# Performance work log

Measured on AMD Instinct MI355X. Metric: run time of the kernel, lower is better.

## Reference

```python
import jax, jax.numpy as jnp
import numpy as np

D = 256; NH = 8; NL = 4; NP = 4; HD = D // NH
SHAPES = np.array([[180, 180], [90, 90], [45, 45], [23, 23]], dtype=np.int32)
LQ = int((SHAPES[:, 0] * SHAPES[:, 1]).sum())  # 43054
STARTS = np.concatenate([[0], np.cumsum(SHAPES[:, 0] * SHAPES[:, 1])[:-1]]).astype(np.int32)


def setup_inputs():
    ks = jax.random.split(jax.random.key(0), 16)
    s = 0.02
    p = lambda k, shp: jax.random.normal(k, shp, jnp.float32) * s
    return {
        "query": jax.random.normal(ks[0], (1, LQ, D), jnp.float32),
        "ref_points": jax.random.uniform(ks[1], (1, LQ, NL, 2), dtype=jnp.float32),
        "pos": jax.random.normal(ks[2], (1, LQ, D), jnp.float32),
        "input_spatial_shapes": jnp.asarray(SHAPES),
        "input_level_start_index": jnp.asarray(STARTS),
        "w_off": p(ks[3], (D, NH * NL * NP * 2)), "b_off": p(ks[4], (NH * NL * NP * 2,)),
        "w_attn": p(ks[5], (D, NH * NL * NP)), "b_attn": p(ks[6], (NH * NL * NP,)),
        "w_val": p(ks[7], (D, D)), "b_val": jnp.zeros((D,), jnp.float32),
        "w_out": p(ks[8], (D, D)), "b_out": jnp.zeros((D,), jnp.float32),
        "g1": jnp.ones((D,), jnp.float32), "beta1": jnp.zeros((D,), jnp.float32),
        "w1": p(ks[9], (D, D)), "b1": jnp.zeros((D,), jnp.float32),
        "w2": p(ks[10], (D, D)), "b2": jnp.zeros((D,), jnp.float32),
        "g2": jnp.ones((D,), jnp.float32), "beta2": jnp.zeros((D,), jnp.float32),
    }


def _ln(x, g, b):
    m = x.mean(-1, keepdims=True)
    v = ((x - m) ** 2).mean(-1, keepdims=True)
    return (x - m) * jax.lax.rsqrt(v + 1e-5) * g + b


def _sample_level(v, Hl, Wl, loc):
    # v: (B, Hl*Wl, NH, HD); loc: (B, Lq, NH, NP, 2) normalized to [0,1]
    # Bilinear sampling matching F.grid_sample(align_corners=False, padding_mode='zeros')
    B, _, nh, d = v.shape
    Lq, P = loc.shape[1], loc.shape[3]
    vb = jnp.transpose(v, (0, 2, 1, 3))  # (B, NH, HW, d)
    x = loc[..., 0] * Wl - 0.5
    y = loc[..., 1] * Hl - 0.5
    x0 = jnp.floor(x); y0 = jnp.floor(y)
    fx = x - x0; fy = y - y0
    out = jnp.zeros((B, nh, Lq, P, d), v.dtype)
    for dy in (0, 1):
        for dx in (0, 1):
            xi = x0 + dx; yi = y0 + dy
            w = (fx if dx else 1.0 - fx) * (fy if dy else 1.0 - fy)
            valid = (xi >= 0) & (xi < Wl) & (yi >= 0) & (yi < Hl)
            xc = jnp.clip(xi, 0, Wl - 1).astype(jnp.int32)
            yc = jnp.clip(yi, 0, Hl - 1).astype(jnp.int32)
            idx = jnp.transpose(yc * Wl + xc, (0, 2, 1, 3)).reshape(B, nh, Lq * P)
            g = jnp.take_along_axis(vb, idx[..., None], axis=2).reshape(B, nh, Lq, P, d)
            wt = jnp.transpose(jnp.where(valid, w, 0.0), (0, 2, 1, 3))
            out = out + g * wt[..., None]
    return out  # (B, NH, Lq, NP, HD)


def _layer(query, ref_points, pos, shp, sti, w_off, b_off, w_attn, b_attn, w_val, b_val,
           w_out, b_out, g1, beta1, w1, b1, w2, b2, g2, beta2):
    B, Lq, _ = query.shape
    q = query + pos  # with_pos_embed
    value = (query @ w_val + b_val).reshape(B, Lq, NH, HD)
    off = (q @ w_off + b_off).reshape(B, Lq, NH, NL, NP, 2)
    aw = jax.nn.softmax((q @ w_attn + b_attn).reshape(B, Lq, NH, NL * NP), axis=-1)
    aw = aw.reshape(B, Lq, NH, NL, NP)
    # offset_normalizer = [W_l, H_l]
    norm = jnp.asarray(shp[:, ::-1].copy(), jnp.float32)
    loc = ref_points[:, :, None, :, None, :] + off / norm[None, None, None, :, None, :]
    acc = jnp.zeros((B, NH, Lq, HD), query.dtype)
    for l in range(NL):
        Hl, Wl = int(shp[l, 0]), int(shp[l, 1])
        st = int(sti[l])
        sampled = _sample_level(value[:, st:st + Hl * Wl], Hl, Wl, loc[:, :, :, l])
        wl = jnp.transpose(aw[:, :, :, l], (0, 2, 1, 3))  # (B, NH, Lq, NP)
        acc = acc + (sampled * wl[..., None]).sum(axis=3)
    attn_out = acc.transpose(0, 2, 1, 3).reshape(B, Lq, D) @ w_out + b_out
    # residual + LayerNorm + FFN (dropout is identity in eval mode)
    x = _ln(query + attn_out, g1, beta1)
    ffn = jax.nn.relu(x @ w1 + b1) @ w2 + b2
    return _ln(x + ffn, g2, beta2)


def reference(query, ref_points, pos, input_spatial_shapes, input_level_start_index,
              w_off, b_off, w_attn, b_attn, w_val, b_val, w_out, b_out,
              g1, beta1, w1, b1, w2, b2, g2, beta2):
    shp = np.asarray(input_spatial_shapes)
    sti = np.asarray(input_level_start_index)
    return _layer(query, ref_points, pos, shp, sti, w_off, b_off, w_attn, b_attn,
                  w_val, b_val, w_out, b_out, g1, beta1, w1, b1, w2, b2, g2, beta2)
```

## Files before the change

kernel.cpp:

```cpp
#include <hip/hip_runtime.h>

typedef unsigned short u16;
typedef unsigned int u32;
typedef float f32x4 __attribute__((ext_vector_type(4)));
typedef short i16x8 __attribute__((ext_vector_type(8)));
typedef __bf16 bf16x8_t __attribute__((ext_vector_type(8)));

#define LQ 43054

__device__ __forceinline__ float bf2f(u16 u) {
  union { u32 i; float f; } v; v.i = ((u32)u) << 16; return v.f;
}
__device__ __forceinline__ u16 f2bf(float f) {
  u32 i = __float_as_uint(f);
  return (u16)((i + 0x7FFFu + ((i >> 16) & 1u)) >> 16);
}

__device__ __forceinline__ float dot2bf(u32 v, u32 w, float c) {
  float d;
  asm("v_dot2_f32_bf16 %0, %1, %2, %3" : "=v"(d) : "v"(v), "v"(w), "v"(c));
  return d;
}

template <typename T>
__device__ __forceinline__ auto mfma_try(T a, T b, f32x4 c, int)
    -> decltype(__builtin_amdgcn_mfma_f32_16x16x32_bf16(a, b, c, 0, 0, 0)) {
  return __builtin_amdgcn_mfma_f32_16x16x32_bf16(a, b, c, 0, 0, 0);
}
template <typename T>
__device__ __forceinline__ f32x4 mfma_try(T a, T b, f32x4 c, long) {
  return __builtin_amdgcn_mfma_f32_16x16x32_bf16(
      __builtin_bit_cast(bf16x8_t, a), __builtin_bit_cast(bf16x8_t, b), c, 0, 0, 0);
}
__device__ __forceinline__ f32x4 mfma_bf16(i16x8 a, i16x8 b, f32x4 c) {
  return mfma_try(a, b, c, 0);
}

__global__ void transpose_all_kernel(
    const float* __restrict__ w_off, const float* __restrict__ w_attn,
    const float* __restrict__ w_val, const float* __restrict__ w_out,
    const float* __restrict__ w1, const float* __restrict__ w2,
    u16* __restrict__ wT) {
  int b = blockIdx.x;
  const float* src; u16* dst; int N; int col;
  if (b < 256)       { src = w_off;  dst = wT;          N = 256; col = b; }
  else if (b < 384)  { src = w_attn; dst = wT + 65536;  N = 128; col = b - 256; }
  else if (b < 640)  { src = w_val;  dst = wT + 98304;  N = 256; col = b - 384; }
  else if (b < 896)  { src = w_out;  dst = wT + 163840; N = 256; col = b - 640; }
  else if (b < 1152) { src = w1;     dst = wT + 229376; N = 256; col = b - 896; }
  else               { src = w2;     dst = wT + 294912; N = 256; col = b - 1152; }
  dst[col * 256 + threadIdx.x] = f2bf(src[threadIdx.x * N + col]);
}

__device__ __forceinline__ void stage_a_dma(uint4* As, const u16* A, int r0, int M,
                                            int w, int lane) {
#pragma unroll
  for (int jj = 0; jj < 8; ++jj) {
    int row = w * 16 + jj * 2 + (lane >> 5);
    int gr = min(r0 + row, M - 1);
    int c = lane & 31;
    const uint4* gp = (const uint4*)A + (size_t)gr * 32 + (c ^ (row & 7));
    __builtin_amdgcn_global_load_lds(
        (const __attribute__((address_space(1))) void*)gp,
        (__attribute__((address_space(3))) void*)(As + (w * 16 + jj * 2) * 32),
        16, 0, 0);
  }
}
template <int ADD, int PH>
__device__ __forceinline__ void stage_a_f32(uint4* As, const float* A, const float* A2,
                                            int r0, int M, int tid) {
  constexpr int IT = 16 / PH;
#pragma unroll
  for (int h = 0; h < PH; ++h) {
    float4 va[IT];
    float4 vp[ADD ? IT : 1];
#pragma unroll
    for (int it = 0; it < IT; ++it) {
      int e = tid + (h * IT + it) * 256;
      int gr = min(r0 + (e >> 6), M - 1);
      int idx = gr * 64 + (e & 63);
      va[it] = ((const float4*)A)[idx];
      if constexpr (ADD) vp[it] = ((const float4*)A2)[idx];
    }
#pragma unroll
    for (int it = 0; it < IT; ++it) {
      int e = tid + (h * IT + it) * 256;
      int row = e >> 6, c4 = e & 63;
      float4 v = va[it];
      if constexpr (ADD) {
        v.x += vp[it].x; v.y += vp[it].y; v.z += vp[it].z; v.w += vp[it].w;
      }
      uint2 pk;
      pk.x = (u32)f2bf(v.x) | ((u32)f2bf(v.y) << 16);
      pk.y = (u32)f2bf(v.z) | ((u32)f2bf(v.w) << 16);
      int c = c4 >> 1, hf = c4 & 1;
      ((uint2*)As)[((row * 32 + (c ^ (row & 7))) << 1) | hf] = pk;
    }
  }
}
__device__ __forceinline__ void load_b(i16x8* f, const u16* Bt, int t, int l16, int quad) {
  const uint4* bp = (const uint4*)Bt + (t * 16 + l16) * 32 + quad;
#pragma unroll
  for (int kk = 0; kk < 8; ++kk) f[kk] = __builtin_bit_cast(i16x8, bp[kk << 2]);
}
__device__ __forceinline__ void tile_mfma(f32x4* acc, const uint4* As,
                                          const i16x8* bfr, int l16, int quad) {
#pragma unroll
  for (int rg = 0; rg < 4; ++rg) {
    int arow = rg * 16 + l16;
    f32x4 a = {0.f, 0.f, 0.f, 0.f};
#pragma unroll
    for (int kk = 0; kk < 8; ++kk) {
      i16x8 afr = __builtin_bit_cast(i16x8, As[arow * 32 + (((kk << 2) + quad) ^ (arow & 7))]);
      a = mfma_bf16(afr, bfr[kk], a);
    }
    acc[rg] = a;
  }
}

#define LS_STRIDE 264
__device__ __forceinline__ void lds_store_rows(const u16* Ls, u16* out,
                                               int r0, int M, int w, int lane) {
#pragma unroll
  for (int it = 0; it < 8; ++it) {
    int lrow = w * 16 + it * 2 + (lane >> 5);
    int grow = r0 + lrow;
    int chunk = lane & 31;
    if (grow < M) {
      *(uint4*)(out + (size_t)grow * 256 + chunk * 8) =
          *(const uint4*)(Ls + lrow * LS_STRIDE + chunk * 8);
    }
  }
}

template <int AIN, int MODE>
__global__ __launch_bounds__(256, 3) void gemm_kernel(
    const void* __restrict__ Av, const u16* __restrict__ Bt,
    const float* __restrict__ bias, void* __restrict__ out, int M) {
  __shared__ uint4 As[2176];
  const int tid = threadIdx.x;
  const int w = tid >> 6, lane = tid & 63, quad = lane >> 4, l16 = lane & 15;
  const int r0 = blockIdx.x * 64;
  if constexpr (AIN == 2) stage_a_dma(As, (const u16*)Av, r0, M, w, lane);
  else                    stage_a_f32<0, 2>(As, (const float*)Av, nullptr, r0, M, tid);
  __syncthreads();
  i16x8 bfr[2][8];
  load_b(bfr[0], Bt, w * 4, l16, quad);
  f32x4 vals[4][4];
#pragma unroll
  for (int i = 0; i < 4; ++i) {
    const int t = w * 4 + i;
    if (i + 1 < 4) load_b(bfr[(i + 1) & 1], Bt, t + 1, l16, quad);
    tile_mfma(vals[i], As, bfr[i & 1], l16, quad);
  }
  __syncthreads();
  u16* Ls = (u16*)As;
#pragma unroll
  for (int i = 0; i < 4; ++i) {
    const int col = (w * 4 + i) * 16 + l16;
    const float bv = bias[col];
#pragma unroll
    for (int rg = 0; rg < 4; ++rg)
#pragma unroll
      for (int r = 0; r < 4; ++r) {
        float v = vals[i][rg][r] + bv;
        if (MODE == 2) v = fmaxf(v, 0.f);
        Ls[(rg * 16 + (quad << 2) + r) * LS_STRIDE + col] = f2bf(v);
      }
  }
  __syncthreads();
  lds_store_rows(Ls, (u16*)out, r0, M, w, lane);
}

__global__ __launch_bounds__(256, 3) void offaw_gemm_kernel(
    const float* __restrict__ query, const float* __restrict__ pos,
    const u16* __restrict__ Bt, const float* __restrict__ b_off,
    const float* __restrict__ b_attn, u16* __restrict__ offb,
    float* __restrict__ aw, int M) {
  __shared__ uint4 As[2176];
  const int tid = threadIdx.x;
  const int w = tid >> 6, lane = tid & 63, quad = lane >> 4, l16 = lane & 15;
  const int r0 = blockIdx.x * 64;
  stage_a_f32<1, 4>(As, query, pos, r0, M, tid);
  __syncthreads();
  i16x8 bfr[2][8];
  load_b(bfr[0], Bt, w, l16, quad);
  f32x4 vals[4][4];
#pragma unroll
  for (int i = 0; i < 6; ++i) {
    const int t = w + 4 * i;
    if (i + 1 < 6) load_b(bfr[(i + 1) & 1], Bt, w + 4 * (i + 1), l16, quad);
    if (i < 4) {
      tile_mfma(vals[i], As, bfr[i & 1], l16, quad);
    } else {
      f32x4 acc[4];
      tile_mfma(acc, As, bfr[i & 1], l16, quad);
      const int colc = (t - 16) * 16 + l16;
      const float bv = b_attn[colc];
#pragma unroll
      for (int rg = 0; rg < 4; ++rg)
#pragma unroll
        for (int r = 0; r < 4; ++r) {
          float v = acc[rg][r] + bv;
          float m = v;
#pragma unroll
          for (int o = 1; o < 16; o <<= 1) m = fmaxf(m, __shfl_xor(m, o));
          float e = __expf(v - m);
          float s = e;
#pragma unroll
          for (int o = 1; o < 16; o <<= 1) s += __shfl_xor(s, o);
          int row = r0 + rg * 16 + (quad << 2) + r;
          if (row < M) aw[row * 128 + colc] = e / s;
        }
    }
  }
  __syncthreads();
  u16* Ls = (u16*)As;
#pragma unroll
  for (int i = 0; i < 4; ++i) {
    const int col = (w + 4 * i) * 16 + l16;
    const float bv = b_off[col];
#pragma unroll
    for (int rg = 0; rg < 4; ++rg)
#pragma unroll
      for (int r = 0; r < 4; ++r)
        Ls[(rg * 16 + (quad << 2) + r) * LS_STRIDE + col] = f2bf(vals[i][rg][r] + bv);
  }
  __syncthreads();
  lds_store_rows(Ls, offb, r0, M, w, lane);
}

template <int RBF, int OBF>
__global__ __launch_bounds__(256, 2) void gemm_ln_kernel(
    const u16* __restrict__ A, const u16* __restrict__ Bt,
    const float* __restrict__ bias, const void* __restrict__ residv,
    const float* __restrict__ g, const float* __restrict__ beta,
    void* __restrict__ outv, int M) {
  __shared__ uint4 As[2176];
  __shared__ float2 pnorm[256];
  const int tid = threadIdx.x;
  const int w = tid >> 6, lane = tid & 63, quad = lane >> 4, l16 = lane & 15;
  const int r0 = blockIdx.x * 64;
  stage_a_dma(As, A, r0, M, w, lane);
  __syncthreads();
  i16x8 bfr[2][8];
  load_b(bfr[0], Bt, w * 4, l16, quad);
  f32x4 vals[4][4];
#pragma unroll
  for (int i = 0; i < 4; ++i) {
    const int t = w * 4 + i;
    if (i + 1 < 4) load_b(bfr[(i + 1) & 1], Bt, t + 1, l16, quad);
    tile_mfma(vals[i], As, bfr[i & 1], l16, quad);
  }
  float s[16], s2[16];
#pragma unroll
  for (int k = 0; k < 16; ++k) { s[k] = 0.f; s2[k] = 0.f; }
#pragma unroll
  for (int i = 0; i < 4; ++i) {
    const int col = (w * 4 + i) * 16 + l16;
    const float bv = bias[col];
#pragma unroll
    for (int rg = 0; rg < 4; ++rg)
#pragma unroll
      for (int r = 0; r < 4; ++r) {
        int row = r0 + rg * 16 + (quad << 2) + r;
        float rv = 0.f;
        if (row < M) rv = RBF ? bf2f(((const u16*)residv)[row * 256 + col])
                              : ((const float*)residv)[row * 256 + col];
        float v = vals[i][rg][r] + bv + rv;
        vals[i][rg][r] = v;
        s[rg * 4 + r] += v; s2[rg * 4 + r] += v * v;
      }
  }
#pragma unroll
  for (int k = 0; k < 16; ++k)
#pragma unroll
    for (int o = 1; o < 16; o <<= 1) {
      s[k] += __shfl_xor(s[k], o);
      s2[k] += __shfl_xor(s2[k], o);
    }
  if (l16 == 0) {
#pragma unroll
    for (int rg = 0; rg < 4; ++rg)
#pragma unroll
      for (int r = 0; r < 4; ++r) {
        int lrow = rg * 16 + (quad << 2) + r;
        pnorm[lrow * 4 + w] = make_float2(s[rg * 4 + r], s2[rg * 4 + r]);
      }
  }
  __syncthreads();
  if constexpr (OBF) {
    u16* Ls = (u16*)As;
#pragma unroll
    for (int rg = 0; rg < 4; ++rg)
#pragma unroll
      for (int r = 0; r < 4; ++r) {
        int lrow = rg * 16 + (quad << 2) + r;
        float4 p01 = ((const float4*)pnorm)[lrow * 2];
        float4 p23 = ((const float4*)pnorm)[lrow * 2 + 1];
        float ss = p01.x + p01.z + p23.x + p23.z;
        float qq = p01.y + p01.w + p23.y + p23.w;
        float mean = ss * (1.f / 256.f);
        float var = qq * (1.f / 256.f) - mean * mean;
        float inv = rsqrtf(var + 1e-5f);
#pragma unroll
        for (int i = 0; i < 4; ++i) {
          const int col = (w * 4 + i) * 16 + l16;
          float o = (vals[i][rg][r] - mean) * inv * g[col] + beta[col];
          Ls[lrow * LS_STRIDE + col] = f2bf(o);
        }
      }
    __syncthreads();
    lds_store_rows(Ls, (u16*)outv, r0, M, w, lane);
  } else {
#pragma unroll
    for (int rg = 0; rg < 4; ++rg)
#pragma unroll
      for (int r = 0; r < 4; ++r) {
        int lrow = rg * 16 + (quad << 2) + r;
        float4 p01 = ((const float4*)pnorm)[lrow * 2];
        float4 p23 = ((const float4*)pnorm)[lrow * 2 + 1];
        float ss = p01.x + p01.z + p23.x + p23.z;
        float qq = p01.y + p01.w + p23.y + p23.w;
        float mean = ss * (1.f / 256.f);
        float var = qq * (1.f / 256.f) - mean * mean;
        float inv = rsqrtf(var + 1e-5f);
        int row = r0 + lrow;
        if (row < M) {
#pragma unroll
          for (int i = 0; i < 4; ++i) {
            const int col = (w * 4 + i) * 16 + l16;
            float o = (vals[i][rg][r] - mean) * inv * g[col] + beta[col];
            ((float*)outv)[row * 256 + col] = o;
          }
        }
      }
  }
}

__global__ __launch_bounds__(256) void sampler_kernel(
    const float* __restrict__ refp, const u16* __restrict__ offb,
    const float* __restrict__ aw, const u16* __restrict__ value,
    u32* __restrict__ accv) {
  __shared__ uint4 rec[272];
  const int t = threadIdx.x;
  const int b = blockIdx.x;
  {
    const int qs = t >> 7, j = t & 127;
    const int i = b * 2 + qs;
    const int h = j >> 4, lp = j & 15, l = lp >> 2;
    const int Wl = (l == 0) ? 180 : (l == 1) ? 90 : (l == 2) ? 45 : 23;
    const int st = (l == 0) ? 0 : (l == 1) ? 32400 : (l == 2) ? 40500 : 42525;
    const float wj = aw[i * 128 + j];
    const u32 o2 = *(const u32*)(offb + i * 256 + h * 32 + lp * 2);
    const float ox = bf2f((u16)(o2 & 0xffffu)), oy = bf2f((u16)(o2 >> 16));
    const float rx = refp[i * 8 + l * 2], ry = refp[i * 8 + l * 2 + 1];
    float x = rx * (float)Wl + ox - 0.5f;
    float y = ry * (float)Wl + oy - 0.5f;
    float x0f = floorf(x), y0f = floorf(y);
    float fx = x - x0f, fy = y - y0f;
    int x0 = (int)x0f, y0 = (int)y0f;
    bool vx0 = (x0 >= 0) & (x0 < Wl), vx1 = (x0 + 1 >= 0) & (x0 + 1 < Wl);
    bool vy0 = (y0 >= 0) & (y0 < Wl), vy1 = (y0 + 1 >= 0) & (y0 + 1 < Wl);
    int x0c = min(max(x0, 0), Wl - 1), x1c = min(max(x0 + 1, 0), Wl - 1);
    int y0c = min(max(y0, 0), Wl - 1), y1c = min(max(y0 + 1, 0), Wl - 1);
    float w00 = (vx0 & vy0) ? wj * (1.f - fx) * (1.f - fy) : 0.f;
    float w01 = (vx1 & vy0) ? wj * fx * (1.f - fy) : 0.f;
    float w10 = (vx0 & vy1) ? wj * (1.f - fx) * fy : 0.f;
    float w11 = (vx1 & vy1) ? wj * fx * fy : 0.f;
    uint4 r;
    r.x = (u32)((st + y0c * Wl + x0c) * 512 + h * 64) | (u32)(x1c - x0c);
    r.y = (u32)(y1c - y0c) * (u32)(Wl * 512);
    r.z = (u32)f2bf(w00) | ((u32)f2bf(w01) << 16);
    r.w = (u32)f2bf(w10) | ((u32)f2bf(w11) << 16);
    rec[qs * 136 + h * 17 + lp] = r;
  }
  __syncthreads();
  const int qs = t >> 7, j = t & 127;
  const int h = j >> 4, dp = j & 15;
  const char* vb = (const char*)value;
  float a0 = 0.f, a1 = 0.f;
  const int rbase = qs * 136 + h * 17;
  const u32 dp4 = (u32)(dp * 4);
#pragma unroll
  for (int p = 0; p < 16; ++p) {
    uint4 r = rec[rbase + p];
    u32 base = (r.x & 0xFFFFFFFEu) + dp4;
    u32 dxo = (r.x & 1u) << 9;
    u32 dyo = r.y;
    u32 p00 = *(const u32*)(vb + base);
    u32 p01 = *(const u32*)(vb + base + dxo);
    u32 p10 = *(const u32*)(vb + base + dyo);
    u32 p11 = *(const u32*)(vb + base + dyo + dxo);
    a0 = dot2bf(__builtin_amdgcn_perm(p01, p00, 0x05040100u), r.z, a0);
    a1 = dot2bf(__builtin_amdgcn_perm(p01, p00, 0x07060302u), r.z, a1);
    a0 = dot2bf(__builtin_amdgcn_perm(p11, p10, 0x05040100u), r.w, a0);
    a1 = dot2bf(__builtin_amdgcn_perm(p11, p10, 0x07060302u), r.w, a1);
  }
  u32 pk = (u32)f2bf(a0) | ((u32)f2bf(a1) << 16);
  accv[(b * 2 + qs) * 128 + j] = pk;
}

extern "C" void kernel_launch(void* const* d_in, const int* in_sizes, int n_in,
                              void* d_out, int out_size, void* d_ws, size_t ws_size,
                              hipStream_t stream) {
  const float* query  = (const float*)d_in[0];
  const float* refp   = (const float*)d_in[1];
  const float* pos    = (const float*)d_in[2];
  const float* w_off  = (const float*)d_in[5];
  const float* b_off  = (const float*)d_in[6];
  const float* w_attn = (const float*)d_in[7];
  const float* b_attn = (const float*)d_in[8];
  const float* w_val  = (const float*)d_in[9];
  const float* b_val  = (const float*)d_in[10];
  const float* w_out  = (const float*)d_in[11];
  const float* b_out  = (const float*)d_in[12];
  const float* g1     = (const float*)d_in[13];
  const float* beta1  = (const float*)d_in[14];
  const float* w1     = (const float*)d_in[15];
  const float* b1     = (const float*)d_in[16];
  const float* w2     = (const float*)d_in[17];
  const float* b2     = (const float*)d_in[18];
  const float* g2     = (const float*)d_in[19];
  const float* beta2  = (const float*)d_in[20];

  char* ws = (char*)d_ws;
  u16*   wT    = (u16*)(ws + 0);
  u16*   value = (u16*)(ws + 720896);
  u16*   offb  = (u16*)(ws + 22764544);
  float* aw    = (float*)(ws + 44808192);
  u16*   accb  = (u16*)(ws + 66851840);
  u16*   xb    = (u16*)(ws + 720896);
  u16*   hb    = (u16*)(ws + 22764544);

  u16* woffT  = wT;
  u16* wvalT  = wT + 98304;
  u16* woutT  = wT + 163840;
  u16* w1T    = wT + 229376;
  u16* w2T    = wT + 294912;

  transpose_all_kernel<<<1408, 256, 0, stream>>>(w_off, w_attn, w_val, w_out, w1, w2, wT);

  const int gm = (LQ + 63) / 64;
  gemm_kernel<0, 1><<<gm, 256, 0, stream>>>(query, wvalT, b_val, value, LQ);
  offaw_gemm_kernel<<<gm, 256, 0, stream>>>(query, pos, woffT, b_off, b_attn, offb, aw, LQ);
  sampler_kernel<<<LQ / 2, 256, 0, stream>>>(refp, offb, aw, value, (u32*)accb);
  gemm_ln_kernel<0, 1><<<gm, 256, 0, stream>>>(accb, woutT, b_out, query, g1, beta1, xb, LQ);
  gemm_kernel<2, 2><<<gm, 256, 0, stream>>>(xb, w1T, b1, hb, LQ);
  gemm_ln_kernel<1, 0><<<gm, 256, 0, stream>>>(hb, w2T, b2, xb, g2, beta2, d_out, LQ);
}
```

Baseline: 419.3 us.

## Fuse output projection, LayerNorms and FFN into one kernel; widen sampler per-thread work

Three tail kernels (out-proj+LN1, FFN1, FFN2+LN2) become one kernel per 64-row tile. The LN1 output and the FFN hidden activations stay in swizzled LDS instead of going through global memory, which removes two launches and the intermediate bf16 round trips. The sampler now handles 4 queries per block, with each thread gathering 8-byte chunks into 4 accumulators. It also remaps block indices so neighbouring queries land on the same XCD. The costs are higher LDS use (two 32KB buffers), which may lower occupancy, and more register pressure in both kernels.

```diff
diff --git a/kernel.cpp b/kernel.cpp
--- a/kernel.cpp
+++ b/kernel.cpp
@@ -118,6 +118,10 @@
   }
 }
 
+__device__ __forceinline__ int swz_u16(int row, int col) {
+  return row * 256 + ((((col >> 3) ^ (row & 7)) << 3) | (col & 7));
+}
+
 #define LS_STRIDE 264
 __device__ __forceinline__ void lds_store_rows(const u16* Ls, u16* out,
                                                int r0, int M, int w, int lane) {
@@ -230,43 +234,44 @@
   lds_store_rows(Ls, offb, r0, M, w, lane);
 }
 
-template <int RBF, int OBF>
-__global__ __launch_bounds__(256, 2) void gemm_ln_kernel(
-    const u16* __restrict__ A, const u16* __restrict__ Bt,
-    const float* __restrict__ bias, const void* __restrict__ residv,
-    const float* __restrict__ g, const float* __restrict__ beta,
-    void* __restrict__ outv, int M) {
-  __shared__ uint4 As[2176];
+__global__ __launch_bounds__(256, 2) void tail_fused_kernel(
+    const u16* __restrict__ accb, const u16* __restrict__ woutT,
+    const float* __restrict__ b_out, const float* __restrict__ query,
+    const float* __restrict__ g1, const float* __restrict__ beta1,
+    const u16* __restrict__ w1T, const float* __restrict__ b1,
+    const u16* __restrict__ w2T, const float* __restrict__ b2,
+    const float* __restrict__ g2, const float* __restrict__ beta2,
+    float* __restrict__ out, int M) {
+  __shared__ uint4 As[2048];
+  __shared__ uint4 Xs[2048];
   __shared__ float2 pnorm[256];
   const int tid = threadIdx.x;
   const int w = tid >> 6, lane = tid & 63, quad = lane >> 4, l16 = lane & 15;
   const int r0 = blockIdx.x * 64;
-  stage_a_dma(As, A, r0, M, w, lane);
+  stage_a_dma(As, accb, r0, M, w, lane);
   __syncthreads();
   i16x8 bfr[2][8];
-  load_b(bfr[0], Bt, w * 4, l16, quad);
   f32x4 vals[4][4];
-#pragma unroll
-  for (int i = 0; i < 4; ++i) {
-    const int t = w * 4 + i;
-    if (i + 1 < 4) load_b(bfr[(i + 1) & 1], Bt, t + 1, l16, quad);
+  float s[16], s2[16];
+
+  load_b(bfr[0], woutT, w * 4, l16, quad);
+#pragma unroll
+  for (int i = 0; i < 4; ++i) {
+    if (i + 1 < 4) load_b(bfr[(i + 1) & 1], woutT, w * 4 + i + 1, l16, quad);
     tile_mfma(vals[i], As, bfr[i & 1], l16, quad);
   }
-  float s[16], s2[16];
 #pragma unroll
   for (int k = 0; k < 16; ++k) { s[k] = 0.f; s2[k] = 0.f; }
 #pragma unroll
   for (int i = 0; i < 4; ++i) {
     const int col = (w * 4 + i) * 16 + l16;
-    const float bv = bias[col];
+    const float bv = b_out[col];
 #pragma unroll
     for (int rg = 0; rg < 4; ++rg)
 #pragma unroll
       for (int r = 0; r < 4; ++r) {
         int row = r0 + rg * 16 + (quad << 2) + r;
-        float rv = 0.f;
-        if (row < M) rv = RBF ? bf2f(((const u16*)residv)[row * 256 + col])
-                              : ((const float*)residv)[row * 256 + col];
+        float rv = (row < M) ? query[row * 256 + col] : 0.f;
         float v = vals[i][rg][r] + bv + rv;
         vals[i][rg][r] = v;
         s[rg * 4 + r] += v; s2[rg * 4 + r] += v * v;
@@ -283,122 +288,190 @@
 #pragma unroll
     for (int rg = 0; rg < 4; ++rg)
 #pragma unroll
+      for (int r = 0; r < 4; ++r)
+        pnorm[(rg * 16 + (quad << 2) + r) * 4 + w] = make_float2(s[rg * 4 + r], s2[rg * 4 + r]);
+  }
+  __syncthreads();
+  u16* Xu = (u16*)Xs;
+#pragma unroll
+  for (int rg = 0; rg < 4; ++rg)
+#pragma unroll
+    for (int r = 0; r < 4; ++r) {
+      int lrow = rg * 16 + (quad << 2) + r;
+      float4 p01 = ((const float4*)pnorm)[lrow * 2];
+      float4 p23 = ((const float4*)pnorm)[lrow * 2 + 1];
+      float ss = p01.x + p01.z + p23.x + p23.z;
+      float qq = p01.y + p01.w + p23.y + p23.w;
+      float mean = ss * (1.f / 256.f);
+      float var = qq * (1.f / 256.f) - mean * mean;
+      float inv = rsqrtf(var + 1e-5f);
+#pragma unroll
+      for (int i = 0; i < 4; ++i) {
+        const int col = (w * 4 + i) * 16 + l16;
+        float o = (vals[i][rg][r] - mean) * inv * g1[col] + beta1[col];
+        Xu[swz_u16(lrow, col)] = f2bf(o);
+      }
+    }
+  __syncthreads();
+
+  load_b(bfr[0], w1T, w * 4, l16, quad);
+#pragma unroll
+  for (int i = 0; i < 4; ++i) {
+    if (i + 1 < 4) load_b(bfr[(i + 1) & 1], w1T, w * 4 + i + 1, l16, quad);
+    tile_mfma(vals[i], Xs, bfr[i & 1], l16, quad);
+  }
+  u16* Hu = (u16*)As;
+#pragma unroll
+  for (int i = 0; i < 4; ++i) {
+    const int col = (w * 4 + i) * 16 + l16;
+    const float bv = b1[col];
+#pragma unroll
+    for (int rg = 0; rg < 4; ++rg)
+#pragma unroll
       for (int r = 0; r < 4; ++r) {
         int lrow = rg * 16 + (quad << 2) + r;
-        pnorm[lrow * 4 + w] = make_float2(s[rg * 4 + r], s2[rg * 4 + r]);
-      }
-  }
-  __syncthreads();
-  if constexpr (OBF) {
-    u16* Ls = (u16*)As;
+        Hu[swz_u16(lrow, col)] = f2bf(fmaxf(vals[i][rg][r] + bv, 0.f));
+      }
+  }
+  __syncthreads();
+
+  load_b(bfr[0], w2T, w * 4, l16, quad);
+#pragma unroll
+  for (int i = 0; i < 4; ++i) {
+    if (i + 1 < 4) load_b(bfr[(i + 1) & 1], w2T, w * 4 + i + 1, l16, quad);
+    tile_mfma(vals[i], As, bfr[i & 1], l16, quad);
+  }
+#pragma unroll
+  for (int k = 0; k < 16; ++k) { s[k] = 0.f; s2[k] = 0.f; }
+#pragma unroll
+  for (int i = 0; i < 4; ++i) {
+    const int col = (w * 4 + i) * 16 + l16;
+    const float bv = b2[col];
 #pragma unroll
     for (int rg = 0; rg < 4; ++rg)
 #pragma unroll
       for (int r = 0; r < 4; ++r) {
         int lrow = rg * 16 + (quad << 2) + r;
-        float4 p01 = ((const float4*)pnorm)[lrow * 2];
-        float4 p23 = ((const float4*)pnorm)[lrow * 2 + 1];
-        float ss = p01.x + p01.z + p23.x + p23.z;
-        float qq = p01.y + p01.w + p23.y + p23.w;
-        float mean = ss * (1.f / 256.f);
-        float var = qq * (1.f / 256.f) - mean * mean;
-        float inv = rsqrtf(var + 1e-5f);
+        float xv = bf2f(Xu[swz_u16(lrow, col)]);
+        float v = vals[i][rg][r] + bv + xv;
+        vals[i][rg][r] = v;
+        s[rg * 4 + r] += v; s2[rg * 4 + r] += v * v;
+      }
+  }
+#pragma unroll
+  for (int k = 0; k < 16; ++k)
+#pragma unroll
+    for (int o = 1; o < 16; o <<= 1) {
+      s[k] += __shfl_xor(s[k], o);
+      s2[k] += __shfl_xor(s2[k], o);
+    }
+  if (l16 == 0) {
+#pragma unroll
+    for (int rg = 0; rg < 4; ++rg)
+#pragma unroll
+      for (int r = 0; r < 4; ++r)
+        pnorm[(rg * 16 + (quad << 2) + r) * 4 + w] = make_float2(s[rg * 4 + r], s2[rg * 4 + r]);
+  }
+  __syncthreads();
+#pragma unroll
+  for (int rg = 0; rg < 4; ++rg)
+#pragma unroll
+    for (int r = 0; r < 4; ++r) {
+      int lrow = rg * 16 + (quad << 2) + r;
+      float4 p01 = ((const float4*)pnorm)[lrow * 2];
+      float4 p23 = ((const float4*)pnorm)[lrow * 2 + 1];
+      float ss = p01.x + p01.z + p23.x + p23.z;
+      float qq = p01.y + p01.w + p23.y + p23.w;
+      float mean = ss * (1.f / 256.f);
+      float var = qq * (1.f / 256.f) - mean * mean;
+      float inv = rsqrtf(var + 1e-5f);
+      int row = r0 + lrow;
+      if (row < M) {
 #pragma unroll
         for (int i = 0; i < 4; ++i) {
           const int col = (w * 4 + i) * 16 + l16;
-          float o = (vals[i][rg][r] - mean) * inv * g[col] + beta[col];
-          Ls[lrow * LS_STRIDE + col] = f2bf(o);
+          out[row * 256 + col] = (vals[i][rg][r] - mean) * inv * g2[col] + beta2[col];
         }
       }
-    __syncthreads();
-    lds_store_rows(Ls, (u16*)outv, r0, M, w, lane);
-  } else {
-#pragma unroll
-    for (int rg = 0; rg < 4; ++rg)
-#pragma unroll
-      for (int r = 0; r < 4; ++r) {
-        int lrow = rg * 16 + (quad << 2) + r;
-        float4 p01 = ((const float4*)pnorm)[lrow * 2];
-        float4 p23 = ((const float4*)pnorm)[lrow * 2 + 1];
-        float ss = p01.x + p01.z + p23.x + p23.z;
-        float qq = p01.y + p01.w + p23.y + p23.w;
-        float mean = ss * (1.f / 256.f);
-        float var = qq * (1.f / 256.f) - mean * mean;
-        float inv = rsqrtf(var + 1e-5f);
-        int row = r0 + lrow;
-        if (row < M) {
-#pragma unroll
-          for (int i = 0; i < 4; ++i) {
-            const int col = (w * 4 + i) * 16 + l16;
-            float o = (vals[i][rg][r] - mean) * inv * g[col] + beta[col];
-            ((float*)outv)[row * 256 + col] = o;
-          }
-        }
-      }
-  }
+    }
 }
 
 __global__ __launch_bounds__(256) void sampler_kernel(
     const float* __restrict__ refp, const u16* __restrict__ offb,
     const float* __restrict__ aw, const u16* __restrict__ value,
     u32* __restrict__ accv) {
-  __shared__ uint4 rec[272];
+  __shared__ uint4 rec[544];
   const int t = threadIdx.x;
-  const int b = blockIdx.x;
-  {
-    const int qs = t >> 7, j = t & 127;
-    const int i = b * 2 + qs;
-    const int h = j >> 4, lp = j & 15, l = lp >> 2;
-    const int Wl = (l == 0) ? 180 : (l == 1) ? 90 : (l == 2) ? 45 : 23;
-    const int st = (l == 0) ? 0 : (l == 1) ? 32400 : (l == 2) ? 40500 : 42525;
-    const float wj = aw[i * 128 + j];
-    const u32 o2 = *(const u32*)(offb + i * 256 + h * 32 + lp * 2);
-    const float ox = bf2f((u16)(o2 & 0xffffu)), oy = bf2f((u16)(o2 >> 16));
-    const float rx = refp[i * 8 + l * 2], ry = refp[i * 8 + l * 2 + 1];
-    float x = rx * (float)Wl + ox - 0.5f;
-    float y = ry * (float)Wl + oy - 0.5f;
-    float x0f = floorf(x), y0f = floorf(y);
-    float fx = x - x0f, fy = y - y0f;
-    int x0 = (int)x0f, y0 = (int)y0f;
-    bool vx0 = (x0 >= 0) & (x0 < Wl), vx1 = (x0 + 1 >= 0) & (x0 + 1 < Wl);
-    bool vy0 = (y0 >= 0) & (y0 < Wl), vy1 = (y0 + 1 >= 0) & (y0 + 1 < Wl);
-    int x0c = min(max(x0, 0), Wl - 1), x1c = min(max(x0 + 1, 0), Wl - 1);
-    int y0c = min(max(y0, 0), Wl - 1), y1c = min(max(y0 + 1, 0), Wl - 1);
-    float w00 = (vx0 & vy0) ? wj * (1.f - fx) * (1.f - fy) : 0.f;
-    float w01 = (vx1 & vy0) ? wj * fx * (1.f - fy) : 0.f;
-    float w10 = (vx0 & vy1) ? wj * (1.f - fx) * fy : 0.f;
-    float w11 = (vx1 & vy1) ? wj * fx * fy : 0.f;
-    uint4 r;
-    r.x = (u32)((st + y0c * Wl + x0c) * 512 + h * 64) | (u32)(x1c - x0c);
-    r.y = (u32)(y1c - y0c) * (u32)(Wl * 512);
-    r.z = (u32)f2bf(w00) | ((u32)f2bf(w01) << 16);
-    r.w = (u32)f2bf(w10) | ((u32)f2bf(w11) << 16);
-    rec[qs * 136 + h * 17 + lp] = r;
-  }
-  __syncthreads();
-  const int qs = t >> 7, j = t & 127;
-  const int h = j >> 4, dp = j & 15;
+  const int nwg = gridDim.x;
+  const int qd = nwg >> 3, rm = nwg & 7;
+  const int xcd = blockIdx.x & 7, ii = blockIdx.x >> 3;
+  const int b = (xcd < rm ? xcd * (qd + 1) : rm * (qd + 1) + (xcd - rm) * qd) + ii;
+#pragma unroll
+  for (int it = 0; it < 2; ++it) {
+    const int sidx = t + it * 256;
+    const int qs = sidx >> 7, j = sidx & 127;
+    const int i = b * 4 + qs;
+    if (i < LQ) {
+      const int h = j >> 4, lp = j & 15, l = lp >> 2;
+      const int Wl = (l == 0) ? 180 : (l == 1) ? 90 : (l == 2) ? 45 : 23;
+      const int st = (l == 0) ? 0 : (l == 1) ? 32400 : (l == 2) ? 40500 : 42525;
+      const float wj = aw[i * 128 + j];
+      const u32 o2 = *(const u32*)(offb + i * 256 + h * 32 + lp * 2);
+      const float ox = bf2f((u16)(o2 & 0xffffu)), oy = bf2f((u16)(o2 >> 16));
+      const float rx = refp[i * 8 + l * 2], ry = refp[i * 8 + l * 2 + 1];
+      float x = rx * (float)Wl + ox - 0.5f;
+      float y = ry * (float)Wl + oy - 0.5f;
+      float x0f = floorf(x), y0f = floorf(y);
+      float fx = x - x0f, fy = y - y0f;
+      int x0 = (int)x0f, y0 = (int)y0f;
+      bool vx0 = (x0 >= 0) & (x0 < Wl), vx1 = (x0 + 1 >= 0) & (x0 + 1 < Wl);
+      bool vy0 = (y0 >= 0) & (y0 < Wl), vy1 = (y0 + 1 >= 0) & (y0 + 1 < Wl);
+      int x0c = min(max(x0, 0), Wl - 1), x1c = min(max(x0 + 1, 0), Wl - 1);
+      int y0c = min(max(y0, 0), Wl - 1), y1c = min(max(y0 + 1, 0), Wl - 1);
+      float w00 = (vx0 & vy0) ? wj * (1.f - fx) * (1.f - fy) : 0.f;
+      float w01 = (vx1 & vy0) ? wj * fx * (1.f - fy) : 0.f;
+      float w10 = (vx0 & vy1) ? wj * (1.f - fx) * fy : 0.f;
+      float w11 = (vx1 & vy1) ? wj * fx * fy : 0.f;
+      uint4 r;
+      r.x = (u32)((st + y0c * Wl + x0c) * 512 + h * 64) | (u32)(x1c - x0c);
+      r.y = (u32)(y1c - y0c) * (u32)(Wl * 512);
+      r.z = (u32)f2bf(w00) | ((u32)f2bf(w01) << 16);
+      r.w = (u32)f2bf(w10) | ((u32)f2bf(w11) << 16);
+      rec[qs * 136 + h * 17 + lp] = r;
+    }
+  }
+  __syncthreads();
+  const int qs = t >> 6, j2 = t & 63;
+  const int h = j2 >> 3, dp8 = j2 & 7;
+  const int i = b * 4 + qs;
+  if (i >= LQ) return;
   const char* vb = (const char*)value;
-  float a0 = 0.f, a1 = 0.f;
+  float a0 = 0.f, a1 = 0.f, a2 = 0.f, a3 = 0.f;
   const int rbase = qs * 136 + h * 17;
-  const u32 dp4 = (u32)(dp * 4);
+  const u32 dpo = (u32)(dp8 * 8);
 #pragma unroll
   for (int p = 0; p < 16; ++p) {
     uint4 r = rec[rbase + p];
-    u32 base = (r.x & 0xFFFFFFFEu) + dp4;
+    u32 base = (r.x & 0xFFFFFFFEu) + dpo;
     u32 dxo = (r.x & 1u) << 9;
     u32 dyo = r.y;
-    u32 p00 = *(const u32*)(vb + base);
-    u32 p01 = *(const u32*)(vb + base + dxo);
-    u32 p10 = *(const u32*)(vb + base + dyo);
-    u32 p11 = *(const u32*)(vb + base + dyo + dxo);
-    a0 = dot2bf(__builtin_amdgcn_perm(p01, p00, 0x05040100u), r.z, a0);
-    a1 = dot2bf(__builtin_amdgcn_perm(p01, p00, 0x07060302u), r.z, a1);
-    a0 = dot2bf(__builtin_amdgcn_perm(p11, p10, 0x05040100u), r.w, a0);
-    a1 = dot2bf(__builtin_amdgcn_perm(p11, p10, 0x07060302u), r.w, a1);
-  }
-  u32 pk = (u32)f2bf(a0) | ((u32)f2bf(a1) << 16);
-  accv[(b * 2 + qs) * 128 + j] = pk;
+    uint2 p00 = *(const uint2*)(vb + base);
+    uint2 p01 = *(const uint2*)(vb + base + dxo);
+    uint2 p10 = *(const uint2*)(vb + base + dyo);
+    uint2 p11 = *(const uint2*)(vb + base + dyo + dxo);
+    a0 = dot2bf(__builtin_amdgcn_perm(p01.x, p00.x, 0x05040100u), r.z, a0);
+    a1 = dot2bf(__builtin_amdgcn_perm(p01.x, p00.x, 0x07060302u), r.z, a1);
+    a2 = dot2bf(__builtin_amdgcn_perm(p01.y, p00.y, 0x05040100u), r.z, a2);
+    a3 = dot2bf(__builtin_amdgcn_perm(p01.y, p00.y, 0x07060302u), r.z, a3);
+    a0 = dot2bf(__builtin_amdgcn_perm(p11.x, p10.x, 0x05040100u), r.w, a0);
+    a1 = dot2bf(__builtin_amdgcn_perm(p11.x, p10.x, 0x07060302u), r.w, a1);
+    a2 = dot2bf(__builtin_amdgcn_perm(p11.y, p10.y, 0x05040100u), r.w, a2);
+    a3 = dot2bf(__builtin_amdgcn_perm(p11.y, p10.y, 0x07060302u), r.w, a3);
+  }
+  uint2 pk;
+  pk.x = (u32)f2bf(a0) | ((u32)f2bf(a1) << 16);
+  pk.y = (u32)f2bf(a2) | ((u32)f2bf(a3) << 16);
+  ((uint2*)accv)[i * 64 + h * 8 + dp8] = pk;
 }
 
 extern "C" void kernel_launch(void* const* d_in, const int* in_sizes, int n_in,
@@ -430,8 +503,6 @@
   u16*   offb  = (u16*)(ws + 22764544);
   float* aw    = (float*)(ws + 44808192);
   u16*   accb  = (u16*)(ws + 66851840);
-  u16*   xb    = (u16*)(ws + 720896);
-  u16*   hb    = (u16*)(ws + 22764544);
 
   u16* woffT  = wT;
   u16* wvalT  = wT + 98304;
@@ -444,8 +515,9 @@
   const int gm = (LQ + 63) / 64;
   gemm_kernel<0, 1><<<gm, 256, 0, stream>>>(query, wvalT, b_val, value, LQ);
   offaw_gemm_kernel<<<gm, 256, 0, stream>>>(query, pos, woffT, b_off, b_attn, offb, aw, LQ);
-  sampler_kernel<<<LQ / 2, 256, 0, stream>>>(refp, offb, aw, value, (u32*)accb);
-  gemm_ln_kernel<0, 1><<<gm, 256, 0, stream>>>(accb, woutT, b_out, query, g1, beta1, xb, LQ);
-  gemm_kernel<2, 2><<<gm, 256, 0, stream>>>(xb, w1T, b1, hb, LQ);
-  gemm_ln_kernel<1, 0><<<gm, 256, 0, stream>>>(hb, w2T, b2, xb, g2, beta2, d_out, LQ);
-}
+  const int sb = (LQ + 3) / 4;
+  sampler_kernel<<<sb, 256, 0, stream>>>(refp, offb, aw, value, (u32*)accb);
+  tail_fused_kernel<<<gm, 256, 0, stream>>>(accb, woutT, b_out, query, g1, beta1,
+                                            w1T, b1, w2T, b2, g2, beta2,
+                                            (float*)d_out, LQ);
+}
```

After: 407.5 us. 1.03x faster.
